# Kernel tuning notes

Measured on AMD Instinct MI355X. Metric: run time of the kernel, lower is better.

## Reference

```python
import jax, jax.numpy as jnp
import numpy as np

H = 16
D_MODEL = 1024
B, S = 2, 2048
DH = D_MODEL // H


def setup_inputs() -> dict:
    key = jax.random.key(0)
    ks = jax.random.split(key, 12)
    std = 0.02
    q = jax.random.normal(ks[0], (B, S, D_MODEL), dtype=jnp.float32)
    k = jax.random.normal(ks[1], (B, S, D_MODEL), dtype=jnp.float32)
    v = jax.random.normal(ks[2], (B, S, D_MODEL), dtype=jnp.float32)
    # additive causal mask: 0 on/below diagonal, -1e9 above
    causal = jnp.tril(jnp.ones((S, S), dtype=bool))
    mask = jnp.where(causal, 0.0, -1e9).astype(jnp.float32)[None, None, :, :]
    def dense(kk):
        return (jax.random.normal(kk, (D_MODEL, D_MODEL), dtype=jnp.float32) * std,
                jnp.zeros((D_MODEL,), dtype=jnp.float32))
    Wq, bq = dense(ks[3])
    Wk, bk = dense(ks[4])
    Wv, bv = dense(ks[5])
    Wo, bo = dense(ks[6])
    return {"q": q, "k": k, "v": v, "mask": mask,
            "Wq": Wq, "bq": bq, "Wk": Wk, "bk": bk,
            "Wv": Wv, "bv": bv, "Wo": Wo, "bo": bo}


def reference(q, k, v, mask, Wq, bq, Wk, bk, Wv, bv, Wo, bo):
    b, s, d = q.shape
    def split_heads(x):  # [b,s,d] -> [b,h,s,dh]
        return x.reshape(b, s, H, DH).transpose(0, 2, 1, 3)
    qh = split_heads(q @ Wq + bq)
    kh = split_heads(k @ Wk + bk)
    vh = split_heads(v @ Wv + bv)
    scale = 1.0 / jnp.sqrt(jnp.asarray(DH, dtype=qh.dtype))
    scores = jnp.einsum('bhqd,bhkd->bhqk', qh, kh) * scale + mask
    weights = jax.nn.softmax(scores, axis=-1)
    ctx = jnp.einsum('bhqk,bhkd->bhqd', weights, vh)
    ctx = ctx.transpose(0, 2, 1, 3).reshape(b, s, d)
    return ctx @ Wo + bo
```

## Files before the change

### kernel.cpp

```cpp
#include <hip/hip_runtime.h>
#include <hip/hip_bf16.h>
#include <stdint.h>

typedef __bf16 bf16x8 __attribute__((ext_vector_type(8)));
typedef float  f32x4  __attribute__((ext_vector_type(4)));
typedef __hip_bfloat16 bf16_t;

#define D_MODEL 1024
#define NH 16
#define DH 64
#define BB 2
#define SS 2048
#define MTOT (BB*SS)
#define NQT (SS/64)

#define GBM 128
#define GBN 128
#define GBK 64

__global__ void cvt_qkv_kernel(const float* __restrict__ q, const float* __restrict__ k,
                               const float* __restrict__ v, bf16_t* __restrict__ dst) {
  const int n1v = MTOT * D_MODEL / 4;
  int tid = blockIdx.x * blockDim.x + threadIdx.x;
  int stride = gridDim.x * blockDim.x;
  for (int i = tid; i < 3 * n1v; i += stride) {
    int which = i / n1v;
    int j = i - which * n1v;
    const float4* src = (const float4*)(which == 0 ? q : (which == 1 ? k : v));
    float4 f = src[j];
    union { bf16_t h[4]; short4 s4; } u;
    u.h[0] = __float2bfloat16(f.x);
    u.h[1] = __float2bfloat16(f.y);
    u.h[2] = __float2bfloat16(f.z);
    u.h[3] = __float2bfloat16(f.w);
    ((short4*)dst)[(size_t)which * n1v + j] = u.s4;
  }
}

__global__ void transpose_w_kernel(const float* __restrict__ W0, const float* __restrict__ W1,
                                   const float* __restrict__ W2, const float* __restrict__ W3,
                                   bf16_t* __restrict__ WtAll) {
  __shared__ float tile[32][33];
  const int z = blockIdx.z;
  const float* W = (z == 0) ? W0 : (z == 1) ? W1 : (z == 2) ? W2 : W3;
  bf16_t* Wt = WtAll + (size_t)z * D_MODEL * D_MODEL;
  const int tx = threadIdx.x, ty = threadIdx.y;
  const int bx = blockIdx.x, by = blockIdx.y;
#pragma unroll
  for (int i = 0; i < 4; ++i)
    tile[ty + i * 8][tx] = W[(size_t)(by * 32 + ty + i * 8) * D_MODEL + bx * 32 + tx];
  __syncthreads();
#pragma unroll
  for (int i = 0; i < 4; ++i)
    Wt[(size_t)(bx * 32 + ty + i * 8) * D_MODEL + by * 32 + tx] =
        __float2bfloat16(tile[tx][ty + i * 8]);
}

__device__ __forceinline__ void g2lds16(const bf16_t* g, bf16_t* l) {
  __builtin_amdgcn_global_load_lds((__attribute__((address_space(1))) void*)(g),
                                   (__attribute__((address_space(3))) void*)(l), 16, 0, 0);
}

__device__ __forceinline__ void gemm_tile_mainloop(const bf16_t* __restrict__ A,
                                                   const bf16_t* __restrict__ Bt,
                                                   bf16_t* As, bf16_t* Bs,
                                                   int m0, int n0, f32x4 acc[4][4]) {
  const int tid = threadIdx.x;
  const int wv = tid >> 6, ln = tid & 63;
  const int wr = wv >> 1, wc = wv & 1;
  const int lr = ln & 15, lg = ln >> 4;

#pragma unroll
  for (int mi = 0; mi < 4; ++mi)
#pragma unroll
    for (int ni = 0; ni < 4; ++ni)
      acc[mi][ni] = (f32x4){0.f, 0.f, 0.f, 0.f};

  for (int kt = 0; kt < D_MODEL / GBK; ++kt) {
#pragma unroll
    for (int c = 0; c < 4; ++c) {
      int chunk = wv * 4 + c;
      int row = chunk * 8 + (ln >> 3);
      int col = (ln & 7) * 8;
      g2lds16(A  + (size_t)(m0 + row) * D_MODEL + kt * GBK + col, As + chunk * 8 * GBK);
      g2lds16(Bt + (size_t)(n0 + row) * D_MODEL + kt * GBK + col, Bs + chunk * 8 * GBK);
    }
    __syncthreads();
#pragma unroll
    for (int ks = 0; ks < 2; ++ks) {
      bf16x8 af[4], bfr[4];
#pragma unroll
      for (int mi = 0; mi < 4; ++mi)
        af[mi] = *(const bf16x8*)(As + (size_t)(wr * 64 + mi * 16 + lr) * GBK + ks * 32 + lg * 8);
#pragma unroll
      for (int ni = 0; ni < 4; ++ni)
        bfr[ni] = *(const bf16x8*)(Bs + (size_t)(wc * 64 + ni * 16 + lr) * GBK + ks * 32 + lg * 8);
#pragma unroll
      for (int mi = 0; mi < 4; ++mi)
#pragma unroll
        for (int ni = 0; ni < 4; ++ni)
          acc[mi][ni] = __builtin_amdgcn_mfma_f32_16x16x32_bf16(af[mi], bfr[ni], acc[mi][ni], 0, 0, 0);
    }
    __syncthreads();
  }
}

__global__ __launch_bounds__(256)
void proj_gemm_kernel(const bf16_t* __restrict__ Aq, const bf16_t* __restrict__ Ak,
                      const bf16_t* __restrict__ Av, const bf16_t* __restrict__ WtAll,
                      const float* __restrict__ bq, const float* __restrict__ bk,
                      const float* __restrict__ bv,
                      bf16_t* __restrict__ Qg, bf16_t* __restrict__ Kg,
                      bf16_t* __restrict__ Vt) {
  __shared__ bf16_t As[GBM * GBK];
  __shared__ bf16_t Bs[GBN * GBK];
  const int z = blockIdx.z;
  const bf16_t* A = (z == 0) ? Aq : (z == 1) ? Ak : Av;
  const bf16_t* Bt = WtAll + (size_t)z * D_MODEL * D_MODEL;
  const float* bias = (z == 0) ? bq : (z == 1) ? bk : bv;
  const int m0 = blockIdx.y * GBM, n0 = blockIdx.x * GBN;

  f32x4 acc[4][4];
  gemm_tile_mainloop(A, Bt, As, Bs, m0, n0, acc);

  const int tid = threadIdx.x;
  const int wv = tid >> 6, ln = tid & 63;
  const int wr = wv >> 1, wc = wv & 1;
  const int lr = ln & 15, lg = ln >> 4;

#pragma unroll
  for (int mi = 0; mi < 4; ++mi) {
#pragma unroll
    for (int ni = 0; ni < 4; ++ni) {
      int ncol = n0 + wc * 64 + ni * 16 + lr;
      float bsv = bias[ncol];
#pragma unroll
      for (int j = 0; j < 4; ++j) {
        int mrow = m0 + wr * 64 + mi * 16 + lg * 4 + j;
        bf16_t hv = __float2bfloat16(acc[mi][ni][j] + bsv);
        if (z == 0) {
          Qg[(size_t)mrow * D_MODEL + ncol] = hv;
        } else if (z == 1) {
          Kg[(size_t)mrow * D_MODEL + ncol] = hv;
        } else {
          int b = mrow >> 11, s = mrow & (SS - 1);
          Vt[(size_t)((b << 10) | ncol) * SS + s] = hv;
        }
      }
    }
  }
}

__global__ __launch_bounds__(256)
void out_gemm_kernel(const bf16_t* __restrict__ Ctx, const bf16_t* __restrict__ Wto,
                     const float* __restrict__ bo, float* __restrict__ out) {
  __shared__ bf16_t As[GBM * GBK];
  __shared__ bf16_t Bs[GBN * GBK];
  const int m0 = blockIdx.y * GBM, n0 = blockIdx.x * GBN;

  f32x4 acc[4][4];
  gemm_tile_mainloop(Ctx, Wto, As, Bs, m0, n0, acc);

  const int tid = threadIdx.x;
  const int wv = tid >> 6, ln = tid & 63;
  const int wr = wv >> 1, wc = wv & 1;
  const int lr = ln & 15, lg = ln >> 4;

#pragma unroll
  for (int mi = 0; mi < 4; ++mi) {
#pragma unroll
    for (int ni = 0; ni < 4; ++ni) {
      int ncol = n0 + wc * 64 + ni * 16 + lr;
      float bsv = bo[ncol];
#pragma unroll
      for (int j = 0; j < 4; ++j) {
        int mrow = m0 + wr * 64 + mi * 16 + lg * 4 + j;
        out[(size_t)mrow * D_MODEL + ncol] = acc[mi][ni][j] + bsv;
      }
    }
  }
}

__device__ __forceinline__ void attn_run(
    f32x4 acc_o[2][4], f32x4 acc_l[2], float m_run[2][4],
    const bf16x8 qf[2][2], const bf16_t* Kbase, const bf16_t* Vbase,
    bf16_t (*P)[72], int q0, int t0, int t1, int lr, int lg, bf16x8 onesf) {
  bf16x8 kf_cur[2][4];
#pragma unroll
  for (int ks = 0; ks < 2; ++ks)
#pragma unroll
    for (int kb = 0; kb < 4; ++kb)
      kf_cur[ks][kb] = *(const bf16x8*)(Kbase + (size_t)(t0 * 64 + kb * 16 + lr) * D_MODEL + ks * 32 + lg * 8);

  for (int t = t0; t < t1; ++t) {
    const int kv0 = t * 64;
    f32x4 sc[2][4];
#pragma unroll
    for (int mi = 0; mi < 2; ++mi)
#pragma unroll
      for (int kb = 0; kb < 4; ++kb) sc[mi][kb] = (f32x4){0.f, 0.f, 0.f, 0.f};

    __builtin_amdgcn_s_setprio(1);
#pragma unroll
    for (int ks = 0; ks < 2; ++ks) {
#pragma unroll
      for (int kb = 0; kb < 4; ++kb) {
        sc[0][kb] = __builtin_amdgcn_mfma_f32_16x16x32_bf16(qf[0][ks], kf_cur[ks][kb], sc[0][kb], 0, 0, 0);
        sc[1][kb] = __builtin_amdgcn_mfma_f32_16x16x32_bf16(qf[1][ks], kf_cur[ks][kb], sc[1][kb], 0, 0, 0);
      }
    }
    __builtin_amdgcn_s_setprio(0);

    bf16x8 kf_nxt[2][4];
    if (t + 1 < t1) {
#pragma unroll
      for (int ks = 0; ks < 2; ++ks)
#pragma unroll
        for (int kb = 0; kb < 4; ++kb)
          kf_nxt[ks][kb] = *(const bf16x8*)(Kbase + (size_t)(kv0 + 64 + kb * 16 + lr) * D_MODEL + ks * 32 + lg * 8);
    }
    bf16x8 vf[2][4];
#pragma unroll
    for (int ks = 0; ks < 2; ++ks)
#pragma unroll
      for (int db = 0; db < 4; ++db)
        vf[ks][db] = *(const bf16x8*)(Vbase + (size_t)(db * 16 + lr) * SS + kv0 + ks * 32 + lg * 8);

    if (kv0 + 63 > q0) {
#pragma unroll
      for (int mi = 0; mi < 2; ++mi)
#pragma unroll
        for (int kb = 0; kb < 4; ++kb)
#pragma unroll
          for (int j = 0; j < 4; ++j) {
            int kc = kv0 + kb * 16 + lr;
            int qr = q0 + mi * 16 + lg * 4 + j;
            if (kc > qr) sc[mi][kb][j] = -1e30f;
          }
    }

#pragma unroll
    for (int mi = 0; mi < 2; ++mi) {
#pragma unroll
      for (int j = 0; j < 4; ++j) {
        float vmax = fmaxf(fmaxf(sc[mi][0][j], sc[mi][1][j]), fmaxf(sc[mi][2][j], sc[mi][3][j]));
#pragma unroll
        for (int off = 1; off < 16; off <<= 1) vmax = fmaxf(vmax, __shfl_xor(vmax, off, 64));
        float mo = m_run[mi][j];
        float mn = fmaxf(mo, vmax);
        float scl = __expf(mo - mn);
        m_run[mi][j] = mn;
#pragma unroll
        for (int kb = 0; kb < 4; ++kb) {
          float p = __expf(sc[mi][kb][j] - mn);
          P[mi * 16 + lg * 4 + j][kb * 16 + lr] = __float2bfloat16(p);
        }
        acc_l[mi][j] *= scl;
#pragma unroll
        for (int db = 0; db < 4; ++db) acc_o[mi][db][j] *= scl;
      }
    }

    asm volatile("s_waitcnt lgkmcnt(0)" ::: "memory");
    __builtin_amdgcn_sched_barrier(0);

    __builtin_amdgcn_s_setprio(1);
#pragma unroll
    for (int ks = 0; ks < 2; ++ks) {
      bf16x8 pa0 = *(const bf16x8*)(&P[lr][ks * 32 + lg * 8]);
      bf16x8 pa1 = *(const bf16x8*)(&P[16 + lr][ks * 32 + lg * 8]);
      acc_l[0] = __builtin_amdgcn_mfma_f32_16x16x32_bf16(pa0, onesf, acc_l[0], 0, 0, 0);
      acc_l[1] = __builtin_amdgcn_mfma_f32_16x16x32_bf16(pa1, onesf, acc_l[1], 0, 0, 0);
#pragma unroll
      for (int db = 0; db < 4; ++db) {
        acc_o[0][db] = __builtin_amdgcn_mfma_f32_16x16x32_bf16(pa0, vf[ks][db], acc_o[0][db], 0, 0, 0);
        acc_o[1][db] = __builtin_amdgcn_mfma_f32_16x16x32_bf16(pa1, vf[ks][db], acc_o[1][db], 0, 0, 0);
      }
    }
    __builtin_amdgcn_s_setprio(0);

    if (t + 1 < t1) {
#pragma unroll
      for (int ks = 0; ks < 2; ++ks)
#pragma unroll
        for (int kb = 0; kb < 4; ++kb)
          kf_cur[ks][kb] = kf_nxt[ks][kb];
    }
  }
}

__device__ __forceinline__ void attn_load_q(bf16x8 qf[2][2], const bf16_t* Qbase,
                                            int q0, int lr, int lg) {
#pragma unroll
  for (int mi = 0; mi < 2; ++mi)
#pragma unroll
    for (int ks = 0; ks < 2; ++ks) {
      bf16x8 raw = *(const bf16x8*)(Qbase + (size_t)(q0 + mi * 16 + lr) * D_MODEL + ks * 32 + lg * 8);
#pragma unroll
      for (int j = 0; j < 8; ++j) raw[j] = (__bf16)((float)raw[j] * 0.125f);
      qf[mi][ks] = raw;
    }
}

__device__ __forceinline__ void attn_init(f32x4 acc_o[2][4], f32x4 acc_l[2], float m_run[2][4]) {
#pragma unroll
  for (int mi = 0; mi < 2; ++mi) {
#pragma unroll
    for (int db = 0; db < 4; ++db) acc_o[mi][db] = (f32x4){0.f, 0.f, 0.f, 0.f};
    acc_l[mi] = (f32x4){0.f, 0.f, 0.f, 0.f};
#pragma unroll
    for (int j = 0; j < 4; ++j) m_run[mi][j] = -1e30f;
  }
}

__global__ __launch_bounds__(256)
void attn_kernel(const bf16_t* __restrict__ Qg, const bf16_t* __restrict__ Kg,
                 const bf16_t* __restrict__ Vt, bf16_t* __restrict__ Ctx) {
  __shared__ __align__(16) bf16_t P_lds[4][32][72];
  __shared__ __align__(16) float  O_part[2][32][68];
  __shared__ float  ml_part[2][32][2];
  const int bh = blockIdx.x;
  const int pp = blockIdx.y;
  const int b = bh >> 4, h = bh & 15;
  const int wv = threadIdx.x >> 6, ln = threadIdx.x & 63;
  const int lr = ln & 15, lg = ln >> 4;

  const int qt_lo = pp, qt_hi = NQT - 1 - pp;
  const int h0 = 16 - pp;
  const int rh = wv & 1;

  const size_t qkbase = (size_t)b * SS * D_MODEL + (size_t)h * DH;
  const bf16_t* Qbase = Qg + qkbase;
  const bf16_t* Kbase = Kg + qkbase;
  const bf16_t* Vbase = Vt + (size_t)(bh * 64) * SS;

  bf16x8 onesf;
#pragma unroll
  for (int j = 0; j < 8; ++j) onesf[j] = (__bf16)1.0f;

  bf16x8 qf[2][2];
  f32x4 acc_o[2][4];
  f32x4 acc_l[2];
  float m_run[2][4];
  const int q0_hi = qt_hi * 64 + rh * 32;

  if (wv < 2) {
    const int q0_lo = qt_lo * 64 + rh * 32;
    attn_load_q(qf, Qbase, q0_lo, lr, lg);
    attn_init(acc_o, acc_l, m_run);
    attn_run(acc_o, acc_l, m_run, qf, Kbase, Vbase, P_lds[wv], q0_lo, 0, pp + 1, lr, lg, onesf);
#pragma unroll
    for (int mi = 0; mi < 2; ++mi)
#pragma unroll
      for (int db = 0; db < 4; ++db)
#pragma unroll
        for (int j = 0; j < 4; ++j) {
          int qr = q0_lo + mi * 16 + lg * 4 + j;
          float val = acc_o[mi][db][j] / acc_l[mi][j];
          Ctx[(size_t)(b * SS + qr) * D_MODEL + h * DH + db * 16 + lr] = __float2bfloat16(val);
        }

    attn_load_q(qf, Qbase, q0_hi, lr, lg);
    attn_init(acc_o, acc_l, m_run);
    attn_run(acc_o, acc_l, m_run, qf, Kbase, Vbase, P_lds[wv], q0_hi, 0, h0, lr, lg, onesf);
  } else {
    attn_load_q(qf, Qbase, q0_hi, lr, lg);
    attn_init(acc_o, acc_l, m_run);
    attn_run(acc_o, acc_l, m_run, qf, Kbase, Vbase, P_lds[wv], q0_hi, h0, NQT - pp, lr, lg, onesf);
    const int pidx = wv - 2;
#pragma unroll
    for (int mi = 0; mi < 2; ++mi)
#pragma unroll
      for (int j = 0; j < 4; ++j) {
        int r = mi * 16 + lg * 4 + j;
#pragma unroll
        for (int db = 0; db < 4; ++db)
          O_part[pidx][r][db * 16 + lr] = acc_o[mi][db][j];
        if (lr == 0) {
          ml_part[pidx][r][0] = m_run[mi][j];
          ml_part[pidx][r][1] = acc_l[mi][j];
        }
      }
  }

  __syncthreads();

  if (wv < 2) {
#pragma unroll
    for (int mi = 0; mi < 2; ++mi)
#pragma unroll
      for (int j = 0; j < 4; ++j) {
        int r = mi * 16 + lg * 4 + j;
        float m1 = m_run[mi][j];
        float m2 = ml_part[wv][r][0];
        float mn = fmaxf(m1, m2);
        float a1 = __expf(m1 - mn);
        float a2 = __expf(m2 - mn);
        float l = a1 * acc_l[mi][j] + a2 * ml_part[wv][r][1];
        int qr = q0_hi + r;
#pragma unroll
        for (int db = 0; db < 4; ++db) {
          float val = (a1 * acc_o[mi][db][j] + a2 * O_part[wv][r][db * 16 + lr]) / l;
          Ctx[(size_t)(b * SS + qr) * D_MODEL + h * DH + db * 16 + lr] = __float2bfloat16(val);
        }
      }
  }
}

extern "C" void kernel_launch(void* const* d_in, const int* in_sizes, int n_in,
                              void* d_out, int out_size, void* d_ws, size_t ws_size,
                              hipStream_t stream) {
  const float* q  = (const float*)d_in[0];
  const float* k  = (const float*)d_in[1];
  const float* v  = (const float*)d_in[2];
  const float* bq = (const float*)d_in[5];
  const float* bk = (const float*)d_in[7];
  const float* bv = (const float*)d_in[9];
  const float* bo = (const float*)d_in[11];
  const float* Wq = (const float*)d_in[4];
  const float* Wk = (const float*)d_in[6];
  const float* Wv = (const float*)d_in[8];
  const float* Wo = (const float*)d_in[10];
  float* out = (float*)d_out;

  char* w = (char*)d_ws;
  bf16_t* Aqkv  = (bf16_t*)(w);
  bf16_t* WtAll = (bf16_t*)(w + 25165824);
  bf16_t* Qg    = (bf16_t*)(w + 33554432);
  bf16_t* Kg    = (bf16_t*)(w + 41943040);
  bf16_t* Vt    = (bf16_t*)(w + 50331648);
  bf16_t* Ctx   = (bf16_t*)(w + 58720256);

  cvt_qkv_kernel<<<2048, 256, 0, stream>>>(q, k, v, Aqkv);
  transpose_w_kernel<<<dim3(32, 32, 4), dim3(32, 8), 0, stream>>>(Wq, Wk, Wv, Wo, WtAll);
  proj_gemm_kernel<<<dim3(8, 32, 3), 256, 0, stream>>>(
      Aqkv, Aqkv + (size_t)MTOT * D_MODEL, Aqkv + 2 * (size_t)MTOT * D_MODEL,
      WtAll, bq, bk, bv, Qg, Kg, Vt);
  attn_kernel<<<dim3(32, 16), 256, 0, stream>>>(Qg, Kg, Vt, Ctx);
  out_gemm_kernel<<<dim3(8, 32), 256, 0, stream>>>(
      Ctx, WtAll + 3 * (size_t)D_MODEL * D_MODEL, bo, out);
}
```

Measured before the change: 295.1 us.

## Transpose attention MFMA operands so each lane owns a query row

Swaps the MFMA operand order for QK^T and PV so scores come out transposed. Each lane then holds one query column, and the row max needs two cross-lane shuffles instead of four per row. The per-row running max shrinks to a single scalar per query block, P is written to LDS as packed bf16 pairs with a new stride, and the context output is staged through LDS so each lane stores 16-byte vectors instead of scattered 2-byte writes. The partial-merge buffers use vector f32x4 stores. The price is more index arithmetic and an extra LDS round trip when storing the output.

```diff
diff --git a/kernel.cpp b/kernel.cpp
--- a/kernel.cpp
+++ b/kernel.cpp
@@ -181,10 +181,19 @@
   }
 }
 
+__device__ __forceinline__ uint32_t pack2bf(float a, float b) {
+  union { __hip_bfloat16 h; unsigned short u; } ua, ub;
+  ua.h = __float2bfloat16(a);
+  ub.h = __float2bfloat16(b);
+  return (uint32_t)ua.u | ((uint32_t)ub.u << 16);
+}
+
+#define PSTRIDE 44
+
 __device__ __forceinline__ void attn_run(
-    f32x4 acc_o[2][4], f32x4 acc_l[2], float m_run[2][4],
+    f32x4 acc_o[2][4], f32x4 acc_l[2], float m_run[2],
     const bf16x8 qf[2][2], const bf16_t* Kbase, const bf16_t* Vbase,
-    bf16_t (*P)[72], int q0, int t0, int t1, int lr, int lg, bf16x8 onesf) {
+    uint32_t (*P32)[PSTRIDE], int q0, int t0, int t1, int lr, int lg, bf16x8 onesf) {
   bf16x8 kf_cur[2][4];
 #pragma unroll
   for (int ks = 0; ks < 2; ++ks)
@@ -196,17 +205,17 @@
     const int kv0 = t * 64;
     f32x4 sc[2][4];
 #pragma unroll
-    for (int mi = 0; mi < 2; ++mi)
-#pragma unroll
-      for (int kb = 0; kb < 4; ++kb) sc[mi][kb] = (f32x4){0.f, 0.f, 0.f, 0.f};
+    for (int qi = 0; qi < 2; ++qi)
+#pragma unroll
+      for (int kb = 0; kb < 4; ++kb) sc[qi][kb] = (f32x4){0.f, 0.f, 0.f, 0.f};
 
     __builtin_amdgcn_s_setprio(1);
 #pragma unroll
     for (int ks = 0; ks < 2; ++ks) {
 #pragma unroll
       for (int kb = 0; kb < 4; ++kb) {
-        sc[0][kb] = __builtin_amdgcn_mfma_f32_16x16x32_bf16(qf[0][ks], kf_cur[ks][kb], sc[0][kb], 0, 0, 0);
-        sc[1][kb] = __builtin_amdgcn_mfma_f32_16x16x32_bf16(qf[1][ks], kf_cur[ks][kb], sc[1][kb], 0, 0, 0);
+        sc[0][kb] = __builtin_amdgcn_mfma_f32_16x16x32_bf16(kf_cur[ks][kb], qf[0][ks], sc[0][kb], 0, 0, 0);
+        sc[1][kb] = __builtin_amdgcn_mfma_f32_16x16x32_bf16(kf_cur[ks][kb], qf[1][ks], sc[1][kb], 0, 0, 0);
       }
     }
     __builtin_amdgcn_s_setprio(0);
@@ -228,53 +237,66 @@
 
     if (kv0 + 63 > q0) {
 #pragma unroll
-      for (int mi = 0; mi < 2; ++mi)
+      for (int qi = 0; qi < 2; ++qi) {
+        int qc = q0 + qi * 16 + lr;
 #pragma unroll
         for (int kb = 0; kb < 4; ++kb)
 #pragma unroll
-          for (int j = 0; j < 4; ++j) {
-            int kc = kv0 + kb * 16 + lr;
-            int qr = q0 + mi * 16 + lg * 4 + j;
-            if (kc > qr) sc[mi][kb][j] = -1e30f;
+          for (int r = 0; r < 4; ++r) {
+            int kc = kv0 + kb * 16 + 4 * lg + r;
+            if (kc > qc) sc[qi][kb][r] = -1e30f;
           }
-    }
-
-#pragma unroll
-    for (int mi = 0; mi < 2; ++mi) {
-#pragma unroll
-      for (int j = 0; j < 4; ++j) {
-        float vmax = fmaxf(fmaxf(sc[mi][0][j], sc[mi][1][j]), fmaxf(sc[mi][2][j], sc[mi][3][j]));
-#pragma unroll
-        for (int off = 1; off < 16; off <<= 1) vmax = fmaxf(vmax, __shfl_xor(vmax, off, 64));
-        float mo = m_run[mi][j];
-        float mn = fmaxf(mo, vmax);
-        float scl = __expf(mo - mn);
-        m_run[mi][j] = mn;
-#pragma unroll
-        for (int kb = 0; kb < 4; ++kb) {
-          float p = __expf(sc[mi][kb][j] - mn);
-          P[mi * 16 + lg * 4 + j][kb * 16 + lr] = __float2bfloat16(p);
+      }
+    }
+
+#pragma unroll
+    for (int qi = 0; qi < 2; ++qi) {
+      float vm = sc[qi][0][0];
+#pragma unroll
+      for (int kb = 0; kb < 4; ++kb)
+#pragma unroll
+        for (int r = 0; r < 4; ++r) vm = fmaxf(vm, sc[qi][kb][r]);
+      vm = fmaxf(vm, __shfl_xor(vm, 16, 64));
+      vm = fmaxf(vm, __shfl_xor(vm, 32, 64));
+      float mo = m_run[qi];
+      float mn = fmaxf(mo, vm);
+      float scl = __expf(mo - mn);
+      m_run[qi] = mn;
+#pragma unroll
+      for (int kb = 0; kb < 4; ++kb)
+#pragma unroll
+        for (int hh = 0; hh < 2; ++hh) {
+          float p0 = __expf(sc[qi][kb][2 * hh]     - mn);
+          float p1 = __expf(sc[qi][kb][2 * hh + 1] - mn);
+          P32[qi * 16 + lr][8 * kb + 2 * lg + hh] = pack2bf(p0, p1);
         }
-        acc_l[mi][j] *= scl;
-#pragma unroll
-        for (int db = 0; db < 4; ++db) acc_o[mi][db][j] *= scl;
-      }
+#pragma unroll
+      for (int r = 0; r < 4; ++r) acc_l[qi][r] *= scl;
+#pragma unroll
+      for (int db = 0; db < 4; ++db)
+#pragma unroll
+        for (int r = 0; r < 4; ++r) acc_o[qi][db][r] *= scl;
     }
 
     asm volatile("s_waitcnt lgkmcnt(0)" ::: "memory");
     __builtin_amdgcn_sched_barrier(0);
 
+    bf16x8 pb[2][2];
+#pragma unroll
+    for (int qi = 0; qi < 2; ++qi)
+#pragma unroll
+      for (int ks = 0; ks < 2; ++ks)
+        pb[qi][ks] = *(const bf16x8*)&P32[qi * 16 + lr][16 * ks + 4 * lg];
+
     __builtin_amdgcn_s_setprio(1);
 #pragma unroll
     for (int ks = 0; ks < 2; ++ks) {
-      bf16x8 pa0 = *(const bf16x8*)(&P[lr][ks * 32 + lg * 8]);
-      bf16x8 pa1 = *(const bf16x8*)(&P[16 + lr][ks * 32 + lg * 8]);
-      acc_l[0] = __builtin_amdgcn_mfma_f32_16x16x32_bf16(pa0, onesf, acc_l[0], 0, 0, 0);
-      acc_l[1] = __builtin_amdgcn_mfma_f32_16x16x32_bf16(pa1, onesf, acc_l[1], 0, 0, 0);
-#pragma unroll
-      for (int db = 0; db < 4; ++db) {
-        acc_o[0][db] = __builtin_amdgcn_mfma_f32_16x16x32_bf16(pa0, vf[ks][db], acc_o[0][db], 0, 0, 0);
-        acc_o[1][db] = __builtin_amdgcn_mfma_f32_16x16x32_bf16(pa1, vf[ks][db], acc_o[1][db], 0, 0, 0);
+#pragma unroll
+      for (int qi = 0; qi < 2; ++qi) {
+        acc_l[qi] = __builtin_amdgcn_mfma_f32_16x16x32_bf16(onesf, pb[qi][ks], acc_l[qi], 0, 0, 0);
+#pragma unroll
+        for (int db = 0; db < 4; ++db)
+          acc_o[qi][db] = __builtin_amdgcn_mfma_f32_16x16x32_bf16(vf[ks][db], pb[qi][ks], acc_o[qi][db], 0, 0, 0);
       }
     }
     __builtin_amdgcn_s_setprio(0);
@@ -292,33 +314,56 @@
 __device__ __forceinline__ void attn_load_q(bf16x8 qf[2][2], const bf16_t* Qbase,
                                             int q0, int lr, int lg) {
 #pragma unroll
-  for (int mi = 0; mi < 2; ++mi)
+  for (int qi = 0; qi < 2; ++qi)
 #pragma unroll
     for (int ks = 0; ks < 2; ++ks) {
-      bf16x8 raw = *(const bf16x8*)(Qbase + (size_t)(q0 + mi * 16 + lr) * D_MODEL + ks * 32 + lg * 8);
+      bf16x8 raw = *(const bf16x8*)(Qbase + (size_t)(q0 + qi * 16 + lr) * D_MODEL + ks * 32 + lg * 8);
 #pragma unroll
       for (int j = 0; j < 8; ++j) raw[j] = (__bf16)((float)raw[j] * 0.125f);
-      qf[mi][ks] = raw;
-    }
-}
-
-__device__ __forceinline__ void attn_init(f32x4 acc_o[2][4], f32x4 acc_l[2], float m_run[2][4]) {
-#pragma unroll
-  for (int mi = 0; mi < 2; ++mi) {
-#pragma unroll
-    for (int db = 0; db < 4; ++db) acc_o[mi][db] = (f32x4){0.f, 0.f, 0.f, 0.f};
-    acc_l[mi] = (f32x4){0.f, 0.f, 0.f, 0.f};
-#pragma unroll
-    for (int j = 0; j < 4; ++j) m_run[mi][j] = -1e30f;
+      qf[qi][ks] = raw;
+    }
+}
+
+__device__ __forceinline__ void attn_init(f32x4 acc_o[2][4], f32x4 acc_l[2], float m_run[2]) {
+#pragma unroll
+  for (int qi = 0; qi < 2; ++qi) {
+#pragma unroll
+    for (int db = 0; db < 4; ++db) acc_o[qi][db] = (f32x4){0.f, 0.f, 0.f, 0.f};
+    acc_l[qi] = (f32x4){0.f, 0.f, 0.f, 0.f};
+    m_run[qi] = -1e30f;
+  }
+}
+
+__device__ __forceinline__ void store_ctx_tile(
+    uint32_t (*P32)[PSTRIDE], const f32x4 acc_o[2][4], const f32x4 acc_l[2],
+    bf16_t* __restrict__ Ctx, int b, int h, int q0, int ln, int lr, int lg) {
+#pragma unroll
+  for (int qi = 0; qi < 2; ++qi) {
+    float rl = 1.0f / acc_l[qi][0];
+#pragma unroll
+    for (int db = 0; db < 4; ++db)
+#pragma unroll
+      for (int hh = 0; hh < 2; ++hh)
+        P32[qi * 16 + lr][8 * db + 2 * lg + hh] =
+            pack2bf(acc_o[qi][db][2 * hh] * rl, acc_o[qi][db][2 * hh + 1] * rl);
+  }
+  asm volatile("s_waitcnt lgkmcnt(0)" ::: "memory");
+  __builtin_amdgcn_sched_barrier(0);
+#pragma unroll
+  for (int c = 0; c < 4; ++c) {
+    int row = (ln >> 2) + 16 * (c >> 1);
+    int dwc = (ln & 3) * 4 + 16 * (c & 1);
+    bf16x8 v = *(const bf16x8*)&P32[row][dwc];
+    *(bf16x8*)(Ctx + (size_t)(b * SS + q0 + row) * D_MODEL + h * DH + dwc * 2) = v;
   }
 }
 
 __global__ __launch_bounds__(256)
 void attn_kernel(const bf16_t* __restrict__ Qg, const bf16_t* __restrict__ Kg,
                  const bf16_t* __restrict__ Vt, bf16_t* __restrict__ Ctx) {
-  __shared__ __align__(16) bf16_t P_lds[4][32][72];
-  __shared__ __align__(16) float  O_part[2][32][68];
-  __shared__ float  ml_part[2][32][2];
+  __shared__ __align__(16) uint32_t P32[4][32][PSTRIDE];
+  __shared__ __align__(16) float O_part[2][32][68];
+  __shared__ float ml_part[2][32][2];
   const int bh = blockIdx.x;
   const int pp = blockIdx.y;
   const int b = bh >> 4, h = bh & 15;
@@ -341,69 +386,57 @@
   bf16x8 qf[2][2];
   f32x4 acc_o[2][4];
   f32x4 acc_l[2];
-  float m_run[2][4];
+  float m_run[2];
   const int q0_hi = qt_hi * 64 + rh * 32;
 
   if (wv < 2) {
     const int q0_lo = qt_lo * 64 + rh * 32;
     attn_load_q(qf, Qbase, q0_lo, lr, lg);
     attn_init(acc_o, acc_l, m_run);
-    attn_run(acc_o, acc_l, m_run, qf, Kbase, Vbase, P_lds[wv], q0_lo, 0, pp + 1, lr, lg, onesf);
-#pragma unroll
-    for (int mi = 0; mi < 2; ++mi)
-#pragma unroll
-      for (int db = 0; db < 4; ++db)
-#pragma unroll
-        for (int j = 0; j < 4; ++j) {
-          int qr = q0_lo + mi * 16 + lg * 4 + j;
-          float val = acc_o[mi][db][j] / acc_l[mi][j];
-          Ctx[(size_t)(b * SS + qr) * D_MODEL + h * DH + db * 16 + lr] = __float2bfloat16(val);
-        }
+    attn_run(acc_o, acc_l, m_run, qf, Kbase, Vbase, P32[wv], q0_lo, 0, pp + 1, lr, lg, onesf);
+    store_ctx_tile(P32[wv], acc_o, acc_l, Ctx, b, h, q0_lo, ln, lr, lg);
 
     attn_load_q(qf, Qbase, q0_hi, lr, lg);
     attn_init(acc_o, acc_l, m_run);
-    attn_run(acc_o, acc_l, m_run, qf, Kbase, Vbase, P_lds[wv], q0_hi, 0, h0, lr, lg, onesf);
+    attn_run(acc_o, acc_l, m_run, qf, Kbase, Vbase, P32[wv], q0_hi, 0, h0, lr, lg, onesf);
   } else {
     attn_load_q(qf, Qbase, q0_hi, lr, lg);
     attn_init(acc_o, acc_l, m_run);
-    attn_run(acc_o, acc_l, m_run, qf, Kbase, Vbase, P_lds[wv], q0_hi, h0, NQT - pp, lr, lg, onesf);
+    attn_run(acc_o, acc_l, m_run, qf, Kbase, Vbase, P32[wv], q0_hi, h0, NQT - pp, lr, lg, onesf);
     const int pidx = wv - 2;
 #pragma unroll
-    for (int mi = 0; mi < 2; ++mi)
-#pragma unroll
-      for (int j = 0; j < 4; ++j) {
-        int r = mi * 16 + lg * 4 + j;
-#pragma unroll
-        for (int db = 0; db < 4; ++db)
-          O_part[pidx][r][db * 16 + lr] = acc_o[mi][db][j];
-        if (lr == 0) {
-          ml_part[pidx][r][0] = m_run[mi][j];
-          ml_part[pidx][r][1] = acc_l[mi][j];
-        }
-      }
+    for (int qi = 0; qi < 2; ++qi) {
+#pragma unroll
+      for (int db = 0; db < 4; ++db)
+        *(f32x4*)&O_part[pidx][qi * 16 + lr][16 * db + 4 * lg] = acc_o[qi][db];
+      if (lg == 0) {
+        ml_part[pidx][qi * 16 + lr][0] = m_run[qi];
+        ml_part[pidx][qi * 16 + lr][1] = acc_l[qi][0];
+      }
+    }
   }
 
   __syncthreads();
 
   if (wv < 2) {
 #pragma unroll
-    for (int mi = 0; mi < 2; ++mi)
-#pragma unroll
-      for (int j = 0; j < 4; ++j) {
-        int r = mi * 16 + lg * 4 + j;
-        float m1 = m_run[mi][j];
-        float m2 = ml_part[wv][r][0];
-        float mn = fmaxf(m1, m2);
-        float a1 = __expf(m1 - mn);
-        float a2 = __expf(m2 - mn);
-        float l = a1 * acc_l[mi][j] + a2 * ml_part[wv][r][1];
-        int qr = q0_hi + r;
-#pragma unroll
-        for (int db = 0; db < 4; ++db) {
-          float val = (a1 * acc_o[mi][db][j] + a2 * O_part[wv][r][db * 16 + lr]) / l;
-          Ctx[(size_t)(b * SS + qr) * D_MODEL + h * DH + db * 16 + lr] = __float2bfloat16(val);
-        }
-      }
+    for (int qi = 0; qi < 2; ++qi) {
+      float m1 = m_run[qi];
+      float m2 = ml_part[wv][qi * 16 + lr][0];
+      float mn = fmaxf(m1, m2);
+      float a1 = __expf(m1 - mn);
+      float a2 = __expf(m2 - mn);
+      float l = a1 * acc_l[qi][0] + a2 * ml_part[wv][qi * 16 + lr][1];
+#pragma unroll
+      for (int db = 0; db < 4; ++db) {
+        f32x4 po = *(const f32x4*)&O_part[wv][qi * 16 + lr][16 * db + 4 * lg];
+#pragma unroll
+        for (int r = 0; r < 4; ++r)
+          acc_o[qi][db][r] = a1 * acc_o[qi][db][r] + a2 * po[r];
+      }
+      acc_l[qi] = (f32x4){l, l, l, l};
+    }
+    store_ctx_tile(P32[wv], acc_o, acc_l, Ctx, b, h, q0_hi, ln, lr, lg);
   }
 }
 
```

Result: faster. 286.2 us (-3.0%).
